# Performance work log

Hardware: AMD Instinct MI355X
Metric: run time of the kernel (lower is better)

## Reference

```python
import jax, jax.numpy as jnp
import numpy as np

B, T, C = 4, 2048, 1024
H = 16
HD = C // H

def setup_inputs() -> dict:
    key = jax.random.key(0)
    k1, k2, k3 = jax.random.split(key, 3)
    hidden_states = jax.random.normal(k1, (B, T, C), dtype=jnp.float32)
    qkv_w = jax.random.normal(k2, (3 * C, C), dtype=jnp.float32) * (C ** -0.5)
    qkv_b = jnp.zeros((3 * C,), dtype=jnp.float32)
    o_w = jax.random.normal(k3, (C, C), dtype=jnp.float32) * (C ** -0.5)
    o_b = jnp.zeros((C,), dtype=jnp.float32)
    return {"hidden_states": hidden_states, "qkv_w": qkv_w, "qkv_b": qkv_b,
            "o_w": o_w, "o_b": o_b}

def reference(hidden_states, qkv_w, qkv_b, o_w, o_b):
    b, t, c = hidden_states.shape
    scaling = HD ** -0.5
    # fused QKV projection (torch Linear: x @ W^T + b)
    qkv = jnp.einsum('btc,dc->btd', hidden_states, qkv_w) + qkv_b
    q, k, v = jnp.split(qkv, 3, axis=-1)
    # [B, H, T, HD]
    q = q.reshape(b, t, H, HD).transpose(0, 2, 1, 3)
    k = k.reshape(b, t, H, HD).transpose(0, 2, 1, 3)
    v = v.reshape(b, t, H, HD).transpose(0, 2, 1, 3)
    attn = jnp.einsum('bhqd,bhkd->bhqk', q, k) * scaling
    causal = jnp.tril(jnp.ones((t, t), dtype=bool))
    attn = jnp.where(causal[None, None], attn, -jnp.inf)
    attn = jax.nn.softmax(attn, axis=-1)
    # dropout: eval mode (identity), matching deterministic reference
    out = jnp.einsum('bhqk,bhkd->bhqd', attn, v)
    out = out.transpose(0, 2, 1, 3).reshape(b, t, c)
    out = jnp.einsum('btc,dc->btd', out, o_w) + o_b
    return out
```

## Files before the change

kernel.cpp:

```cpp
#include <hip/hip_runtime.h>
#include <hip/hip_bf16.h>
#include <stdint.h>

#define TLEN 2048
#define NHEAD 16
#define CD 1024
#define HDIM 64

typedef __attribute__((ext_vector_type(4))) float f32x4;
typedef __attribute__((ext_vector_type(8))) short s16x8;
typedef __attribute__((ext_vector_type(8))) unsigned short u16x8;
typedef __attribute__((ext_vector_type(4))) unsigned short u16x4;
typedef __attribute__((ext_vector_type(2))) unsigned int u32x2;

typedef __attribute__((address_space(1))) const unsigned int global_u32;
typedef __attribute__((address_space(3))) unsigned int lds_u32;

__device__ __forceinline__ void gl_lds16(const void* g, void* l) {
  __builtin_amdgcn_global_load_lds((global_u32*)g, (lds_u32*)l, 16, 0, 0);
}

__device__ __forceinline__ unsigned short f2bf(float x) {
  unsigned int u = __float_as_uint(x);
  u += 0x7fffu + ((u >> 16) & 1u);
  return (unsigned short)(u >> 16);
}

__device__ __forceinline__ f32x4 mfma_bf16(s16x8 a, s16x8 b, f32x4 c) {
  return __builtin_amdgcn_mfma_f32_16x16x32_bf16(a, b, c, 0, 0, 0);
}

__global__ __launch_bounds__(256) void cvt_all(
    const float* __restrict__ X, const float* __restrict__ Wq,
    const float* __restrict__ Wo, unsigned short* __restrict__ Xb,
    unsigned short* __restrict__ Wqb, unsigned short* __restrict__ Wob) {
  int blk = blockIdx.x;
  const float* src;
  unsigned short* dst;
  int base;
  if (blk < 4096) { src = X;  dst = Xb;  base = blk; }
  else if (blk < 5632) { src = Wq; dst = Wqb; base = blk - 4096; }
  else { src = Wo; dst = Wob; base = blk - 5632; }
  int i = (base * 256 + threadIdx.x) * 8;
  float4 a = *(const float4*)(src + i);
  float4 b = *(const float4*)(src + i + 4);
  u16x8 o;
  o[0] = f2bf(a.x); o[1] = f2bf(a.y); o[2] = f2bf(a.z); o[3] = f2bf(a.w);
  o[4] = f2bf(b.x); o[5] = f2bf(b.y); o[6] = f2bf(b.z); o[7] = f2bf(b.w);
  *(u16x8*)(dst + i) = o;
}

#define BM 128
#define BN 128
#define BKG 64

template <int SPLIT>
__global__ __launch_bounds__(256) void gemm_bt(
    const unsigned short* __restrict__ A, const unsigned short* __restrict__ Bw,
    const float* __restrict__ bias, float* __restrict__ Cf,
    unsigned short* __restrict__ qk_out, unsigned short* __restrict__ vt_out,
    int M, int N, int K) {
  __shared__ char lds[(BM + BN) * BKG * 2];
  char* aL = lds;
  char* bL = lds + BM * BKG * 2;
  const int tid = threadIdx.x;
  const int w = tid >> 6, l = tid & 63, l15 = l & 15, l4 = l >> 4;
  const int wr = w >> 1, wc = w & 1;

  const int nbx = gridDim.x;
  const int nwg = nbx * gridDim.y;
  int f = blockIdx.y * nbx + blockIdx.x;
  f = (f & 7) * (nwg >> 3) + (f >> 3);
  const int brow = (f / nbx) * BM, bcol = (f % nbx) * BN;

  f32x4 z4 = {0.f, 0.f, 0.f, 0.f};
  f32x4 acc[4][4];
#pragma unroll
  for (int m = 0; m < 4; ++m)
#pragma unroll
    for (int n = 0; n < 4; ++n) acc[m][n] = z4;

  const unsigned short* Ab = A + (size_t)brow * K;
  const unsigned short* Bb = Bw + (size_t)bcol * K;

  for (int k0 = 0; k0 < K; k0 += BKG) {
    __syncthreads();
#pragma unroll
    for (int i = 0; i < 4; ++i) {
      int ch = i * 256 + tid;
      int r = ch >> 3, c = ch & 7;
      int cs = (c ^ (r & 7)) * 8;
      gl_lds16(Ab + (size_t)r * K + k0 + cs, aL + ch * 16);
      gl_lds16(Bb + (size_t)r * K + k0 + cs, bL + ch * 16);
    }
    __syncthreads();
#pragma unroll
    for (int kk = 0; kk < 2; ++kk) {
      s16x8 af[4], bfr[4];
#pragma unroll
      for (int m = 0; m < 4; ++m) {
        int r = wr * 64 + m * 16 + l15;
        af[m] = *(const s16x8*)(aL + r * (BKG * 2) +
                                ((kk * 64 + l4 * 16) ^ ((r & 7) << 4)));
      }
#pragma unroll
      for (int n = 0; n < 4; ++n) {
        int r = wc * 64 + n * 16 + l15;
        bfr[n] = *(const s16x8*)(bL + r * (BKG * 2) +
                                 ((kk * 64 + l4 * 16) ^ ((r & 7) << 4)));
      }
#pragma unroll
      for (int m = 0; m < 4; ++m)
#pragma unroll
        for (int n = 0; n < 4; ++n) acc[m][n] = mfma_bf16(af[m], bfr[n], acc[m][n]);
    }
  }

#pragma unroll
  for (int m = 0; m < 4; ++m) {
    int row0 = brow + wr * 64 + m * 16 + l4 * 4;
#pragma unroll
    for (int n = 0; n < 4; ++n) {
      int col = bcol + wc * 64 + n * 16 + l15;
      float bs = bias[col];
      if (SPLIT == 0) {
#pragma unroll
        for (int r = 0; r < 4; ++r)
          Cf[(size_t)(row0 + r) * N + col] = acc[m][n][r] + bs;
      } else {
        if (col < 2 * CD) {
#pragma unroll
          for (int r = 0; r < 4; ++r)
            qk_out[(size_t)(row0 + r) * (2 * CD) + col] = f2bf(acc[m][n][r] + bs);
        } else {
          int cc = col - 2 * CD;
          int b_ = row0 >> 11;
          int t = row0 & (TLEN - 1);
          u16x4 pk;
#pragma unroll
          for (int r = 0; r < 4; ++r) pk[r] = f2bf(acc[m][n][r] + bs);
          *(u16x4*)(vt_out + (size_t)(b_ * CD + cc) * TLEN + t) = pk;
        }
      }
    }
  }
}

__global__ __launch_bounds__(256) void attn_fwd(
    const unsigned short* __restrict__ qk,
    const unsigned short* __restrict__ vt,
    unsigned short* __restrict__ ctx) {
  __shared__ char k_lds[64 * 128];
  __shared__ char v_lds[64 * 128];

  const int fblk = blockIdx.y * 32 + blockIdx.x;
  const int xcd = fblk & 7;
  const int bhi = (fblk >> 3) & 7;
  const int qi = 31 - (fblk >> 6);
  const int bh = xcd * 8 + bhi;
  const int b = bh >> 4, h = bh & 15;
  const int tid = threadIdx.x;
  const int w = tid >> 6, l = tid & 63, l15 = l & 15, l4 = l >> 4;
  const int nt = qi + 1;

  const unsigned short* Kg = qk + (size_t)b * TLEN * (2 * CD) + CD + h * HDIM;
  const unsigned short* Vg = vt + (size_t)bh * HDIM * TLEN;

  const float SC2 = 0.18033688011112042f;
  char* pw = k_lds + w * 2048;

  const int sw = (l15 & 7) << 4;
  const int c0 = (l4 * 16) ^ sw;
  const int c1 = (64 + l4 * 16) ^ sw;
  const int row128 = l15 * 128;
  const char* prd0 = pw + row128 + c0;
  const char* prd1 = pw + row128 + c1;
  char* pwr0 = pw + row128 + ((0 * 32 + l4 * 8) ^ sw);
  char* pwr1 = pw + row128 + ((1 * 32 + l4 * 8) ^ sw);
  char* pwr2 = pw + row128 + ((2 * 32 + l4 * 8) ^ sw);
  char* pwr3 = pw + row128 + ((3 * 32 + l4 * 8) ^ sw);
  const int ch0 = tid, ch1 = 256 + tid;
  const int ldsoff0 = ch0 * 16, ldsoff1 = ch1 * 16;
  const int r0 = ch0 >> 3, r1 = ch1 >> 3;
  const int cs0 = ((ch0 & 7) ^ (r0 & 7)) * 8;
  const int cs1 = ((ch1 & 7) ^ (r1 & 7)) * 8;
  const int bperm_addr = (l ^ 32) << 2;

  s16x8 onesf;
#pragma unroll
  for (int j = 0; j < 8; ++j) onesf[j] = (short)0x3F80;

  f32x4 z4 = {0.f, 0.f, 0.f, 0.f};

  const unsigned short* qrow =
      qk + (size_t)(b * TLEN + qi * 64 + w * 16 + l15) * (2 * CD) + h * HDIM;
  s16x8 qf0 = *(const s16x8*)(qrow + l4 * 8);
  s16x8 qf1 = *(const s16x8*)(qrow + 32 + l4 * 8);

  f32x4 acc_o[4];
#pragma unroll
  for (int dc = 0; dc < 4; ++dc) acc_o[dc] = z4;
  f32x4 acc_l = z4;
  float m_r = -3.0e38f;

  const char* gk0 = (const char*)Kg + r0 * 4096 + cs0 * 2;
  const char* gk1 = (const char*)Kg + r1 * 4096 + cs1 * 2;
  const char* gv0 = (const char*)Vg + r0 * 4096 + cs0 * 2;
  const char* gv1 = (const char*)Vg + r1 * 4096 + cs1 * 2;

  s16x8 kstg0 = *(const s16x8*)gk0;
  s16x8 kstg1 = *(const s16x8*)gk1;
  s16x8 vstg0 = *(const s16x8*)gv0;
  s16x8 vstg1 = *(const s16x8*)gv1;

  for (int kt = 0; kt < nt; ++kt) {
    __builtin_amdgcn_s_barrier();
    __builtin_amdgcn_sched_barrier(0);
    asm volatile("s_waitcnt vmcnt(0)" ::: "memory");
    *(s16x8*)(k_lds + ldsoff0) = kstg0;
    *(s16x8*)(k_lds + ldsoff1) = kstg1;
    *(s16x8*)(v_lds + ldsoff0) = vstg0;
    *(s16x8*)(v_lds + ldsoff1) = vstg1;
    if (kt + 1 < nt) {
      gk0 += 262144; gk1 += 262144; gv0 += 128; gv1 += 128;
      kstg0 = *(const s16x8*)gk0;
      kstg1 = *(const s16x8*)gk1;
      vstg0 = *(const s16x8*)gv0;
      vstg1 = *(const s16x8*)gv1;
    }
    asm volatile("s_waitcnt lgkmcnt(0)" ::: "memory");
    __builtin_amdgcn_sched_barrier(0);
    __builtin_amdgcn_s_barrier();
    __builtin_amdgcn_sched_barrier(0);

    const char* ka0 = k_lds + row128 + c0;
    const char* ka1 = k_lds + row128 + c1;

    f32x4 s[4];
    __builtin_amdgcn_s_setprio(1);
#pragma unroll
    for (int n = 0; n < 4; ++n) {
      s16x8 kf0 = *(const s16x8*)(ka0 + n * 2048);
      s16x8 kf1 = *(const s16x8*)(ka1 + n * 2048);
      f32x4 z = z4;
      z = mfma_bf16(kf0, qf0, z);
      z = mfma_bf16(kf1, qf1, z);
      s[n] = z;
    }
    __builtin_amdgcn_s_setprio(0);

    if (kt == qi) {
      int ql = w * 16 + l15;
#pragma unroll
      for (int n = 0; n < 4; ++n)
#pragma unroll
        for (int r = 0; r < 4; ++r)
          if ((n * 16 + l4 * 4 + r) > ql) s[n][r] = -3.0e38f;
    }

    float t0 = fmaxf(fmaxf(s[0][0], s[0][1]), fmaxf(s[0][2], s[0][3]));
    float t1 = fmaxf(fmaxf(s[1][0], s[1][1]), fmaxf(s[1][2], s[1][3]));
    float t2 = fmaxf(fmaxf(s[2][0], s[2][1]), fmaxf(s[2][2], s[2][3]));
    float t3 = fmaxf(fmaxf(s[3][0], s[3][1]), fmaxf(s[3][2], s[3][3]));
    float tm = fmaxf(fmaxf(t0, t1), fmaxf(t2, t3));
    tm = fmaxf(tm, __shfl_xor(tm, 16));
    tm = fmaxf(tm, __int_as_float(__builtin_amdgcn_ds_bpermute(
                       bperm_addr, __float_as_int(tm))));

    __builtin_amdgcn_s_barrier();
    __builtin_amdgcn_sched_barrier(0);

    if (!__all((tm - m_r) * SC2 <= 8.0f)) {
      float m_n = fmaxf(m_r, tm);
      float corr = __builtin_amdgcn_exp2f((m_r - m_n) * SC2);
      m_r = m_n;
      *(float*)(pw + 256 + l15 * 4) = corr;
      asm volatile("s_waitcnt lgkmcnt(0)" ::: "memory");
      __builtin_amdgcn_sched_barrier(0);
      float corr4[4];
#pragma unroll
      for (int r = 0; r < 4; ++r)
        corr4[r] = *(const float*)(pw + 256 + (l4 * 4 + r) * 4);
#pragma unroll
      for (int r = 0; r < 4; ++r) {
        acc_l[r] *= corr4[r];
#pragma unroll
        for (int dc = 0; dc < 4; ++dc) acc_o[dc][r] *= corr4[r];
      }
    }

    float msc = m_r * SC2;
#pragma unroll
    for (int n = 0; n < 4; ++n) {
      float p0 = __builtin_amdgcn_exp2f(fmaf(s[n][0], SC2, -msc));
      float p1 = __builtin_amdgcn_exp2f(fmaf(s[n][1], SC2, -msc));
      float p2 = __builtin_amdgcn_exp2f(fmaf(s[n][2], SC2, -msc));
      float p3 = __builtin_amdgcn_exp2f(fmaf(s[n][3], SC2, -msc));
      u32x2 pr;
      pr[0] = (__float_as_uint(p1) & 0xffff0000u) | (__float_as_uint(p0) >> 16);
      pr[1] = (__float_as_uint(p3) & 0xffff0000u) | (__float_as_uint(p2) >> 16);
      char* dst = (n == 0) ? pwr0 : (n == 1) ? pwr1 : (n == 2) ? pwr2 : pwr3;
      *(u32x2*)dst = pr;
    }

    asm volatile("s_waitcnt lgkmcnt(0)" ::: "memory");
    __builtin_amdgcn_sched_barrier(0);

    __builtin_amdgcn_s_setprio(1);
    {
      s16x8 pf0 = *(const s16x8*)prd0;
      s16x8 pf1 = *(const s16x8*)prd1;
      acc_l = mfma_bf16(pf0, onesf, acc_l);
      acc_l = mfma_bf16(pf1, onesf, acc_l);
#pragma unroll
      for (int dc = 0; dc < 4; ++dc) {
        s16x8 vf0 = *(const s16x8*)(v_lds + dc * 2048 + row128 + c0);
        s16x8 vf1 = *(const s16x8*)(v_lds + dc * 2048 + row128 + c1);
        acc_o[dc] = mfma_bf16(pf0, vf0, acc_o[dc]);
        acc_o[dc] = mfma_bf16(pf1, vf1, acc_o[dc]);
      }
    }
    __builtin_amdgcn_s_setprio(0);
  }

#pragma unroll
  for (int r = 0; r < 4; ++r) {
    int qg = qi * 64 + w * 16 + l4 * 4 + r;
    float inv = 1.0f / acc_l[r];
    size_t base = (size_t)(b * TLEN + qg) * CD + h * HDIM;
#pragma unroll
    for (int dc = 0; dc < 4; ++dc)
      ctx[base + dc * 16 + l15] = f2bf(acc_o[dc][r] * inv);
  }
}

extern "C" void kernel_launch(void* const* d_in, const int* in_sizes, int n_in,
                              void* d_out, int out_size, void* d_ws, size_t ws_size,
                              hipStream_t stream) {
  const float* X  = (const float*)d_in[0];
  const float* Wq = (const float*)d_in[1];
  const float* bq = (const float*)d_in[2];
  const float* Wo = (const float*)d_in[3];
  const float* bo = (const float*)d_in[4];
  float* out = (float*)d_out;

  char* ws = (char*)d_ws;
  unsigned short* Xb  = (unsigned short*)ws;
  unsigned short* Wqb = (unsigned short*)(ws + 16777216);
  unsigned short* Wob = (unsigned short*)(ws + 23068672);
  unsigned short* QK  = (unsigned short*)(ws + 25165824);
  unsigned short* Vt  = (unsigned short*)(ws + 58720256);
  unsigned short* Ctx = Xb;

  cvt_all<<<6144, 256, 0, stream>>>(X, Wq, Wo, Xb, Wqb, Wob);

  gemm_bt<1><<<dim3(24, 64), 256, 0, stream>>>(Xb, Wqb, bq, nullptr, QK, Vt,
                                               8192, 3072, 1024);
  attn_fwd<<<dim3(32, 64), 256, 0, stream>>>(QK, Vt, Ctx);
  gemm_bt<0><<<dim3(8, 64), 256, 0, stream>>>(Ctx, Wob, bo, out, nullptr, nullptr,
                                              8192, 1024, 1024);
}
```

Baseline: 172.0 us.

## Process 128-key tiles per iteration in causal attention kernel

Widens the attention key/value tile from 64 to 128 keys per loop iteration, roughly halving the number of iterations and their barriers, LDS staging rounds and softmax reduction passes per query block. The LDS layouts for K, V and the P scratch are reworked and the causal mask is recomputed for the last tile. It also uses v_max3 for the row max, a packed bf16 conversion with rounding for P, and a launch-bounds occupancy hint. In exchange it uses more registers and LDS, and odd query blocks do some extra masked work on the diagonal tile.

Result: slower. 176.9 us (+2.9%).

```diff
diff --git a/kernel.cpp b/kernel.cpp
--- a/kernel.cpp
+++ b/kernel.cpp
@@ -28,6 +28,17 @@
 
 __device__ __forceinline__ f32x4 mfma_bf16(s16x8 a, s16x8 b, f32x4 c) {
   return __builtin_amdgcn_mfma_f32_16x16x32_bf16(a, b, c, 0, 0, 0);
+}
+
+__device__ __forceinline__ float max3f(float a, float b, float c) {
+  float d;
+  asm("v_max3_f32 %0, %1, %2, %3" : "=v"(d) : "v"(a), "v"(b), "v"(c));
+  return d;
+}
+
+__device__ __forceinline__ unsigned int pk2bf(float a, float b) {
+  __hip_bfloat162 h = __float22bfloat162_rn(make_float2(a, b));
+  return *reinterpret_cast<unsigned int*>(&h);
 }
 
 __global__ __launch_bounds__(256) void cvt_all(
@@ -146,12 +157,12 @@
   }
 }
 
-__global__ __launch_bounds__(256) void attn_fwd(
+__global__ __launch_bounds__(256, 4) void attn_fwd(
     const unsigned short* __restrict__ qk,
     const unsigned short* __restrict__ vt,
     unsigned short* __restrict__ ctx) {
-  __shared__ char k_lds[64 * 128];
-  __shared__ char v_lds[64 * 128];
+  __shared__ char k_lds[128 * 128];
+  __shared__ char v_lds[64 * 256];
 
   const int fblk = blockIdx.y * 32 + blockIdx.x;
   const int xcd = fblk & 7;
@@ -161,29 +172,33 @@
   const int b = bh >> 4, h = bh & 15;
   const int tid = threadIdx.x;
   const int w = tid >> 6, l = tid & 63, l15 = l & 15, l4 = l >> 4;
-  const int nt = qi + 1;
+  const int nt = (qi >> 1) + 1;
 
   const unsigned short* Kg = qk + (size_t)b * TLEN * (2 * CD) + CD + h * HDIM;
   const unsigned short* Vg = vt + (size_t)bh * HDIM * TLEN;
 
   const float SC2 = 0.18033688011112042f;
-  char* pw = k_lds + w * 2048;
+  char* pw = k_lds + w * 4096;
 
   const int sw = (l15 & 7) << 4;
-  const int c0 = (l4 * 16) ^ sw;
-  const int c1 = (64 + l4 * 16) ^ sw;
+  const int cA = (l4 * 16) ^ sw;
+  const int cB = (64 + l4 * 16) ^ sw;
   const int row128 = l15 * 128;
-  const char* prd0 = pw + row128 + c0;
-  const char* prd1 = pw + row128 + c1;
-  char* pwr0 = pw + row128 + ((0 * 32 + l4 * 8) ^ sw);
-  char* pwr1 = pw + row128 + ((1 * 32 + l4 * 8) ^ sw);
-  char* pwr2 = pw + row128 + ((2 * 32 + l4 * 8) ^ sw);
-  char* pwr3 = pw + row128 + ((3 * 32 + l4 * 8) ^ sw);
-  const int ch0 = tid, ch1 = 256 + tid;
-  const int ldsoff0 = ch0 * 16, ldsoff1 = ch1 * 16;
-  const int r0 = ch0 >> 3, r1 = ch1 >> 3;
-  const int cs0 = ((ch0 & 7) ^ (r0 & 7)) * 8;
-  const int cs1 = ((ch1 & 7) ^ (r1 & 7)) * 8;
+  const int prow = l15 * 256;
+  int prd[4], pwr[8];
+#pragma unroll
+  for (int kc = 0; kc < 4; ++kc) prd[kc] = prow + ((kc * 64 + l4 * 16) ^ sw);
+#pragma unroll
+  for (int n = 0; n < 8; ++n) pwr[n] = prow + ((n * 32 + l4 * 8) ^ sw);
+  int voff[4];
+#pragma unroll
+  for (int kc = 0; kc < 4; ++kc) voff[kc] = ((kc * 4 + l4) ^ (l15 & 7)) << 4;
+  const int vrow = l15 * 256;
+  const int ldso0 = tid * 16;
+  const char* gkb = (const char*)Kg + (tid >> 3) * 4096 +
+                    (((tid & 7) ^ ((tid >> 3) & 7)) << 4);
+  const char* gvb = (const char*)Vg + (tid >> 4) * 4096 +
+                    (((tid & 15) ^ ((tid >> 4) & 7)) << 4);
   const int bperm_addr = (l ^ 32) << 2;
 
   s16x8 onesf;
@@ -202,44 +217,52 @@
   for (int dc = 0; dc < 4; ++dc) acc_o[dc] = z4;
   f32x4 acc_l = z4;
   float m_r = -3.0e38f;
-
-  const char* gk0 = (const char*)Kg + r0 * 4096 + cs0 * 2;
-  const char* gk1 = (const char*)Kg + r1 * 4096 + cs1 * 2;
-  const char* gv0 = (const char*)Vg + r0 * 4096 + cs0 * 2;
-  const char* gv1 = (const char*)Vg + r1 * 4096 + cs1 * 2;
-
-  s16x8 kstg0 = *(const s16x8*)gk0;
-  s16x8 kstg1 = *(const s16x8*)gk1;
-  s16x8 vstg0 = *(const s16x8*)gv0;
-  s16x8 vstg1 = *(const s16x8*)gv1;
+  const int qg = w * 16 + l15;
+
+  s16x8 kst0 = *(const s16x8*)(gkb);
+  s16x8 kst1 = *(const s16x8*)(gkb + 131072);
+  s16x8 kst2 = *(const s16x8*)(gkb + 262144);
+  s16x8 kst3 = *(const s16x8*)(gkb + 393216);
+  s16x8 vst0 = *(const s16x8*)(gvb);
+  s16x8 vst1 = *(const s16x8*)(gvb + 65536);
+  s16x8 vst2 = *(const s16x8*)(gvb + 131072);
+  s16x8 vst3 = *(const s16x8*)(gvb + 196608);
 
   for (int kt = 0; kt < nt; ++kt) {
     __builtin_amdgcn_s_barrier();
     __builtin_amdgcn_sched_barrier(0);
     asm volatile("s_waitcnt vmcnt(0)" ::: "memory");
-    *(s16x8*)(k_lds + ldsoff0) = kstg0;
-    *(s16x8*)(k_lds + ldsoff1) = kstg1;
-    *(s16x8*)(v_lds + ldsoff0) = vstg0;
-    *(s16x8*)(v_lds + ldsoff1) = vstg1;
+    *(s16x8*)(k_lds + ldso0)         = kst0;
+    *(s16x8*)(k_lds + ldso0 + 4096)  = kst1;
+    *(s16x8*)(k_lds + ldso0 + 8192)  = kst2;
+    *(s16x8*)(k_lds + ldso0 + 12288) = kst3;
+    *(s16x8*)(v_lds + ldso0)         = vst0;
+    *(s16x8*)(v_lds + ldso0 + 4096)  = vst1;
+    *(s16x8*)(v_lds + ldso0 + 8192)  = vst2;
+    *(s16x8*)(v_lds + ldso0 + 12288) = vst3;
     if (kt + 1 < nt) {
-      gk0 += 262144; gk1 += 262144; gv0 += 128; gv1 += 128;
-      kstg0 = *(const s16x8*)gk0;
-      kstg1 = *(const s16x8*)gk1;
-      vstg0 = *(const s16x8*)gv0;
-      vstg1 = *(const s16x8*)gv1;
+      gkb += 524288; gvb += 256;
+      kst0 = *(const s16x8*)(gkb);
+      kst1 = *(const s16x8*)(gkb + 131072);
+      kst2 = *(const s16x8*)(gkb + 262144);
+      kst3 = *(const s16x8*)(gkb + 393216);
+      vst0 = *(const s16x8*)(gvb);
+      vst1 = *(const s16x8*)(gvb + 65536);
+      vst2 = *(const s16x8*)(gvb + 131072);
+      vst3 = *(const s16x8*)(gvb + 196608);
     }
     asm volatile("s_waitcnt lgkmcnt(0)" ::: "memory");
     __builtin_amdgcn_sched_barrier(0);
     __builtin_amdgcn_s_barrier();
     __builtin_amdgcn_sched_barrier(0);
 
-    const char* ka0 = k_lds + row128 + c0;
-    const char* ka1 = k_lds + row128 + c1;
-
-    f32x4 s[4];
+    const char* ka0 = k_lds + row128 + cA;
+    const char* ka1 = k_lds + row128 + cB;
+
+    f32x4 s[8];
     __builtin_amdgcn_s_setprio(1);
 #pragma unroll
-    for (int n = 0; n < 4; ++n) {
+    for (int n = 0; n < 8; ++n) {
       s16x8 kf0 = *(const s16x8*)(ka0 + n * 2048);
       s16x8 kf1 = *(const s16x8*)(ka1 + n * 2048);
       f32x4 z = z4;
@@ -249,20 +272,21 @@
     }
     __builtin_amdgcn_s_setprio(0);
 
-    if (kt == qi) {
-      int ql = w * 16 + l15;
-#pragma unroll
-      for (int n = 0; n < 4; ++n)
+    if (kt == nt - 1) {
+      int kvb = kt * 128 + l4 * 4 - (qi * 64 + qg);
+#pragma unroll
+      for (int n = 0; n < 8; ++n)
 #pragma unroll
         for (int r = 0; r < 4; ++r)
-          if ((n * 16 + l4 * 4 + r) > ql) s[n][r] = -3.0e38f;
-    }
-
-    float t0 = fmaxf(fmaxf(s[0][0], s[0][1]), fmaxf(s[0][2], s[0][3]));
-    float t1 = fmaxf(fmaxf(s[1][0], s[1][1]), fmaxf(s[1][2], s[1][3]));
-    float t2 = fmaxf(fmaxf(s[2][0], s[2][1]), fmaxf(s[2][2], s[2][3]));
-    float t3 = fmaxf(fmaxf(s[3][0], s[3][1]), fmaxf(s[3][2], s[3][3]));
-    float tm = fmaxf(fmaxf(t0, t1), fmaxf(t2, t3));
+          if (kvb + n * 16 + r > 0) s[n][r] = -3.0e38f;
+    }
+
+    float t[8];
+#pragma unroll
+    for (int n = 0; n < 8; ++n)
+      t[n] = fmaxf(max3f(s[n][0], s[n][1], s[n][2]), s[n][3]);
+    float tm = max3f(max3f(t[0], t[1], t[2]), max3f(t[3], t[4], t[5]),
+                     fmaxf(t[6], t[7]));
     tm = fmaxf(tm, __shfl_xor(tm, 16));
     tm = fmaxf(tm, __int_as_float(__builtin_amdgcn_ds_bpermute(
                        bperm_addr, __float_as_int(tm))));
@@ -274,13 +298,13 @@
       float m_n = fmaxf(m_r, tm);
       float corr = __builtin_amdgcn_exp2f((m_r - m_n) * SC2);
       m_r = m_n;
-      *(float*)(pw + 256 + l15 * 4) = corr;
+      *(float*)(pw + l15 * 4) = corr;
       asm volatile("s_waitcnt lgkmcnt(0)" ::: "memory");
       __builtin_amdgcn_sched_barrier(0);
       float corr4[4];
 #pragma unroll
       for (int r = 0; r < 4; ++r)
-        corr4[r] = *(const float*)(pw + 256 + (l4 * 4 + r) * 4);
+        corr4[r] = *(const float*)(pw + (l4 * 4 + r) * 4);
 #pragma unroll
       for (int r = 0; r < 4; ++r) {
         acc_l[r] *= corr4[r];
@@ -291,33 +315,29 @@
 
     float msc = m_r * SC2;
 #pragma unroll
-    for (int n = 0; n < 4; ++n) {
+    for (int n = 0; n < 8; ++n) {
       float p0 = __builtin_amdgcn_exp2f(fmaf(s[n][0], SC2, -msc));
       float p1 = __builtin_amdgcn_exp2f(fmaf(s[n][1], SC2, -msc));
       float p2 = __builtin_amdgcn_exp2f(fmaf(s[n][2], SC2, -msc));
       float p3 = __builtin_amdgcn_exp2f(fmaf(s[n][3], SC2, -msc));
       u32x2 pr;
-      pr[0] = (__float_as_uint(p1) & 0xffff0000u) | (__float_as_uint(p0) >> 16);
-      pr[1] = (__float_as_uint(p3) & 0xffff0000u) | (__float_as_uint(p2) >> 16);
-      char* dst = (n == 0) ? pwr0 : (n == 1) ? pwr1 : (n == 2) ? pwr2 : pwr3;
-      *(u32x2*)dst = pr;
+      pr[0] = pk2bf(p0, p1);
+      pr[1] = pk2bf(p2, p3);
+      *(u32x2*)(pw + pwr[n]) = pr;
     }
 
     asm volatile("s_waitcnt lgkmcnt(0)" ::: "memory");
     __builtin_amdgcn_sched_barrier(0);
 
     __builtin_amdgcn_s_setprio(1);
-    {
-      s16x8 pf0 = *(const s16x8*)prd0;
-      s16x8 pf1 = *(const s16x8*)prd1;
-      acc_l = mfma_bf16(pf0, onesf, acc_l);
-      acc_l = mfma_bf16(pf1, onesf, acc_l);
+#pragma unroll
+    for (int kc = 0; kc < 4; ++kc) {
+      s16x8 pf = *(const s16x8*)(pw + prd[kc]);
+      acc_l = mfma_bf16(pf, onesf, acc_l);
 #pragma unroll
       for (int dc = 0; dc < 4; ++dc) {
-        s16x8 vf0 = *(const s16x8*)(v_lds + dc * 2048 + row128 + c0);
-        s16x8 vf1 = *(const s16x8*)(v_lds + dc * 2048 + row128 + c1);
-        acc_o[dc] = mfma_bf16(pf0, vf0, acc_o[dc]);
-        acc_o[dc] = mfma_bf16(pf1, vf1, acc_o[dc]);
+        s16x8 vf = *(const s16x8*)(v_lds + vrow + dc * 4096 + voff[kc]);
+        acc_o[dc] = mfma_bf16(pf, vf, acc_o[dc]);
       }
     }
     __builtin_amdgcn_s_setprio(0);
@@ -325,9 +345,9 @@
 
 #pragma unroll
   for (int r = 0; r < 4; ++r) {
-    int qg = qi * 64 + w * 16 + l4 * 4 + r;
+    int qgl = qi * 64 + w * 16 + l4 * 4 + r;
     float inv = 1.0f / acc_l[r];
-    size_t base = (size_t)(b * TLEN + qg) * CD + h * HDIM;
+    size_t base = (size_t)(b * TLEN + qgl) * CD + h * HDIM;
 #pragma unroll
     for (int dc = 0; dc < 4; ++dc)
       ctx[base + dc * 16 + l15] = f2bf(acc_o[dc][r] * inv);
```
